# Performance work log

Measured on AMD Instinct MI355X. Metric: run time of the kernel, lower is better.

## Reference

```python
import jax, jax.numpy as jnp
import numpy as np

def setup_inputs() -> dict:
    key = jax.random.key(0)
    ks = jax.random.split(key, 8)
    B, C, H, W = 4, 64, 64, 64
    Cr = C // 8
    s = 1.0 / np.sqrt(C)
    return {
        "x": jax.random.normal(ks[0], (B, C, H, W), jnp.float32),
        "wq": jax.random.normal(ks[1], (Cr, C), jnp.float32) * s,
        "bq": jax.random.normal(ks[2], (Cr,), jnp.float32) * 0.01,
        "wk": jax.random.normal(ks[3], (Cr, C), jnp.float32) * s,
        "bk": jax.random.normal(ks[4], (Cr,), jnp.float32) * 0.01,
        "wv": jax.random.normal(ks[5], (C, C), jnp.float32) * s,
        "bv": jax.random.normal(ks[6], (C,), jnp.float32) * 0.01,
        "gamma": jax.random.normal(ks[7], (1,), jnp.float32) * 0.1,
    }

def reference(x, wq, bq, wk, bk, wv, bv, gamma):
    B, C, H, W = x.shape
    N = H * W
    xf = x.reshape(B, C, N)  # 1x1 conv == pointwise linear over channel dim
    q = jnp.einsum("oc,bcn->bno", wq, xf) + bq[None, None, :]   # (B, N, Cr)
    k = jnp.einsum("oc,bcn->bon", wk, xf) + bk[None, :, None]   # (B, Cr, N)
    v = jnp.einsum("oc,bcn->bon", wv, xf) + bv[None, :, None]   # (B, C, N)
    attn = jnp.einsum("bno,bom->bnm", q, k)                     # (B, N, N)
    attn = jax.nn.softmax(attn, axis=-1)
    out = jnp.einsum("bcm,bnm->bcn", v, attn)                   # (B, C, N)
    out = out.reshape(B, C, H, W)
    return x + gamma[0] * out
```

## Files before the change

### kernel.cpp

```cpp
#include <hip/hip_runtime.h>

#define BB 4
#define CC 64
#define NN 4096

typedef __attribute__((ext_vector_type(8))) short short8;
typedef __attribute__((ext_vector_type(4))) float f32x4;
typedef unsigned short u16;

#define QWS_ELEMS (BB * NN * 8)

__device__ inline u16 f2bf(float x) {
    unsigned u = __float_as_uint(x);
    u = (u + 0x7fffu + ((u >> 16) & 1u)) >> 16;
    return (u16)u;
}

__device__ inline unsigned permpack(float lo, float hi) {
    return __builtin_amdgcn_perm(__float_as_uint(hi), __float_as_uint(lo), 0x07060302);
}

__global__ __launch_bounds__(256) void proj_kernel(
    const float* __restrict__ x,
    const float* __restrict__ wq, const float* __restrict__ bq,
    const float* __restrict__ wk, const float* __restrict__ bk,
    const float* __restrict__ wv, const float* __restrict__ bv,
    u16* __restrict__ ws_u)
{
    u16* qws = ws_u;
    u16* kws = ws_u + QWS_ELEMS;
    u16* vws = ws_u + 2 * QWS_ELEMS;

    const int u   = blockIdx.y;
    const int pix = blockIdx.x * 256 + threadIdx.x;
    const int b   = pix >> 12;
    const int n   = pix & (NN - 1);

    const float* xb = x + ((size_t)b << 18) + n;

    float aq = bq[u], ak = bk[u];
    float av[8];
#pragma unroll
    for (int i = 0; i < 8; ++i) av[i] = bv[8 * u + i];

#pragma unroll 8
    for (int c = 0; c < CC; ++c) {
        const float xv = xb[(size_t)c << 12];
        aq += wq[u * CC + c] * xv;
        ak += wk[u * CC + c] * xv;
#pragma unroll
        for (int i = 0; i < 8; ++i)
            av[i] += wv[(8 * u + i) * CC + c] * xv;
    }

    qws[(size_t)pix * 8 + u] = f2bf(aq);
    kws[(size_t)pix * 8 + u] = f2bf(ak);
#pragma unroll
    for (int i = 0; i < 8; ++i)
        vws[(((size_t)((b << 6) + 8 * u + i)) << 12) + n] = f2bf(av[i]);
}

__global__ __launch_bounds__(256) void attn_kernel(
    const float* __restrict__ x, const float* __restrict__ gamma,
    const u16* __restrict__ ws_u, float* __restrict__ out)
{
    const u16* qws = ws_u;
    const u16* kws = ws_u + QWS_ELEMS;
    const u16* vws = ws_u + 2 * QWS_ELEMS;

    __shared__ u16   v_t[2][CC * 64];
    __shared__ u16   p_t[2][32 * 64];
    __shared__ float l_sh[4][32];

    const int tid  = threadIdx.x;
    const int w    = tid >> 6;
    const int lane = tid & 63;
    const int quad = lane >> 4;
    const int l15  = lane & 15;

    const int b  = blockIdx.y;
    const int qb = blockIdx.x << 5;
    const int bN = b << 12;

    short8 qf0 = {0,0,0,0,0,0,0,0}, qf1 = {0,0,0,0,0,0,0,0};
    if (quad == 0) {
        qf0 = *(const short8*)(qws + (size_t)(bN + qb + l15) * 8);
        qf1 = *(const short8*)(qws + (size_t)(bN + qb + 16 + l15) * 8);
    }

    short8 kf = {0,0,0,0,0,0,0,0};
    if (quad == 0)
        kf = *(const short8*)(kws + (size_t)(bN + (w << 4) + l15) * 8);

    const int c_row = tid >> 2;
    const int m4    = tid & 3;
    const u16* vrow = vws + (((size_t)((b << 6) + c_row)) << 12);
    short8 vpre0 = *(const short8*)(vrow + (m4 << 3));
    short8 vpre1 = *(const short8*)(vrow + 32 + (m4 << 3));

    const int sw  = c_row & 7;
    const int st0 = c_row * 64 + ((m4 ^ sw) << 3);
    const int st1 = c_row * 64 + (((m4 | 4) ^ sw) << 3);

    const int pm8  = (w << 1) + (quad >> 1);
    const int poff = (quad & 1) << 2;
    const int pw0  = l15 * 64        + ((pm8 ^ (l15 & 7)) << 3) + poff;
    const int pw1  = (16 + l15) * 64 + ((pm8 ^ ((16 + l15) & 7)) << 3) + poff;

    const int qc2   = w & 1;
    const int ch    = w >> 1;
    const int prow  = (qc2 << 4) + l15;
    const int crow0 = (ch << 5) + l15;
    const int crow1 = crow0 + 16;
    const int pr0 = prow * 64  + ((quad       ^ (prow & 7))  << 3);
    const int pr1 = prow * 64  + (((4 + quad) ^ (prow & 7))  << 3);
    const int v00 = crow0 * 64 + ((quad       ^ (crow0 & 7)) << 3);
    const int v01 = crow1 * 64 + ((quad       ^ (crow1 & 7)) << 3);
    const int v10 = crow0 * 64 + (((4 + quad) ^ (crow0 & 7)) << 3);
    const int v11 = crow1 * 64 + (((4 + quad) ^ (crow1 & 7)) << 3);

    f32x4 acc0 = {0.f, 0.f, 0.f, 0.f};
    f32x4 acc1 = {0.f, 0.f, 0.f, 0.f};
    float ls0 = 0.f, ls1 = 0.f;

    for (int it = 0; it < 64; ++it) {
        const int buf   = it & 1;
        const int mnext = ((it + 1) & 63) << 6;

        *(short8*)&v_t[buf][st0] = vpre0;
        *(short8*)&v_t[buf][st1] = vpre1;
        vpre0 = *(const short8*)(vrow + mnext + (m4 << 3));
        vpre1 = *(const short8*)(vrow + mnext + 32 + (m4 << 3));

        f32x4 s0 = __builtin_amdgcn_mfma_f32_16x16x32_bf16(
            kf, qf0, (f32x4){0.f,0.f,0.f,0.f}, 0, 0, 0);
        f32x4 s1 = __builtin_amdgcn_mfma_f32_16x16x32_bf16(
            kf, qf1, (f32x4){0.f,0.f,0.f,0.f}, 0, 0, 0);
        if (quad == 0)
            kf = *(const short8*)(kws + (size_t)(bN + mnext + (w << 4) + l15) * 8);

        const float p00 = __expf(s0[0]), p01 = __expf(s0[1]);
        const float p02 = __expf(s0[2]), p03 = __expf(s0[3]);
        const float p10 = __expf(s1[0]), p11 = __expf(s1[1]);
        const float p12 = __expf(s1[2]), p13 = __expf(s1[3]);
        ls0 += (p00 + p01) + (p02 + p03);
        ls1 += (p10 + p11) + (p12 + p13);
        uint2 a, c2;
        a.x  = permpack(p00, p01);  a.y  = permpack(p02, p03);
        c2.x = permpack(p10, p11);  c2.y = permpack(p12, p13);
        *(uint2*)&p_t[buf][pw0] = a;
        *(uint2*)&p_t[buf][pw1] = c2;

        __syncthreads();

        const short8 pf0  = *(const short8*)&p_t[buf][pr0];
        const short8 pf1  = *(const short8*)&p_t[buf][pr1];
        const short8 vf00 = *(const short8*)&v_t[buf][v00];
        const short8 vf01 = *(const short8*)&v_t[buf][v01];
        const short8 vf10 = *(const short8*)&v_t[buf][v10];
        const short8 vf11 = *(const short8*)&v_t[buf][v11];
        acc0 = __builtin_amdgcn_mfma_f32_16x16x32_bf16(pf0, vf00, acc0, 0, 0, 0);
        acc1 = __builtin_amdgcn_mfma_f32_16x16x32_bf16(pf0, vf01, acc1, 0, 0, 0);
        acc0 = __builtin_amdgcn_mfma_f32_16x16x32_bf16(pf1, vf10, acc0, 0, 0, 0);
        acc1 = __builtin_amdgcn_mfma_f32_16x16x32_bf16(pf1, vf11, acc1, 0, 0, 0);
    }

    ls0 += __shfl_xor(ls0, 16, 64); ls0 += __shfl_xor(ls0, 32, 64);
    ls1 += __shfl_xor(ls1, 16, 64); ls1 += __shfl_xor(ls1, 32, 64);
    if (quad == 0) { l_sh[w][l15] = ls0; l_sh[w][16 + l15] = ls1; }
    __syncthreads();

    const int q0 = (qc2 << 4) + (quad << 2);
    float rl[4];
#pragma unroll
    for (int r = 0; r < 4; ++r)
        rl[r] = 1.f / (l_sh[0][q0 + r] + l_sh[1][q0 + r] +
                       l_sh[2][q0 + r] + l_sh[3][q0 + r]);

    const float g = gamma[0];
#pragma unroll
    for (int half = 0; half < 2; ++half) {
        const int c = half ? crow1 : crow0;
        const f32x4 acc = half ? acc1 : acc0;
        const size_t base = (((size_t)((b << 6) + c)) << 12) + qb + q0;
        const float4 xv = *(const float4*)&x[base];
        float4 o;
        o.x = xv.x + g * acc[0] * rl[0];
        o.y = xv.y + g * acc[1] * rl[1];
        o.z = xv.z + g * acc[2] * rl[2];
        o.w = xv.w + g * acc[3] * rl[3];
        *(float4*)&out[base] = o;
    }
}

extern "C" void kernel_launch(void* const* d_in, const int* in_sizes, int n_in,
                              void* d_out, int out_size, void* d_ws, size_t ws_size,
                              hipStream_t stream)
{
    const float* x     = (const float*)d_in[0];
    const float* wq    = (const float*)d_in[1];
    const float* bq    = (const float*)d_in[2];
    const float* wk    = (const float*)d_in[3];
    const float* bk    = (const float*)d_in[4];
    const float* wv    = (const float*)d_in[5];
    const float* bv    = (const float*)d_in[6];
    const float* gamma = (const float*)d_in[7];
    u16*   ws  = (u16*)d_ws;
    float* out = (float*)d_out;

    hipLaunchKernelGGL(proj_kernel, dim3(BB * NN / 256, 8), dim3(256), 0, stream,
                       x, wq, bq, wk, bk, wv, bv, ws);
    hipLaunchKernelGGL(attn_kernel, dim3(NN / 32, BB), dim3(256), 0, stream,
                       x, gamma, ws, out);
}
```

Before: 112.3 us.

## Restructure projection per pixel and load V fragments directly from global in attention

The projection kernel now holds all 64 input channels of a pixel in registers and splits the output channels across the four wavefronts, with one wave doing q/k plus four v channels. This removes the 8x re-read of x across blockIdx.y and lets q/k be written as packed 16-byte stores. The attention kernel moves to 512 threads covering 64 queries, drops the V shared-memory staging and reads MFMA V fragments straight from global memory with a one-iteration prefetch. This raises occupancy pressure and makes V traffic depend on L2 hits rather than LDS reuse.

```diff
diff --git a/kernel.cpp b/kernel.cpp
--- a/kernel.cpp
+++ b/kernel.cpp
@@ -15,7 +15,9 @@
     u = (u + 0x7fffu + ((u >> 16) & 1u)) >> 16;
     return (u16)u;
 }
-
+__device__ inline unsigned pack2rne(float a, float b) {
+    return (unsigned)f2bf(a) | ((unsigned)f2bf(b) << 16);
+}
 __device__ inline unsigned permpack(float lo, float hi) {
     return __builtin_amdgcn_perm(__float_as_uint(hi), __float_as_uint(lo), 0x07060302);
 }
@@ -31,36 +33,63 @@
     u16* kws = ws_u + QWS_ELEMS;
     u16* vws = ws_u + 2 * QWS_ELEMS;
 
-    const int u   = blockIdx.y;
-    const int pix = blockIdx.x * 256 + threadIdx.x;
-    const int b   = pix >> 12;
-    const int n   = pix & (NN - 1);
-
+    const int part = __builtin_amdgcn_readfirstlane(threadIdx.x >> 6);
+    const int pix  = blockIdx.x * 64 + (threadIdx.x & 63);
+    const int b    = pix >> 12;
+    const int n    = pix & (NN - 1);
     const float* xb = x + ((size_t)b << 18) + n;
 
-    float aq = bq[u], ak = bk[u];
-    float av[8];
-#pragma unroll
-    for (int i = 0; i < 8; ++i) av[i] = bv[8 * u + i];
-
-#pragma unroll 8
-    for (int c = 0; c < CC; ++c) {
-        const float xv = xb[(size_t)c << 12];
-        aq += wq[u * CC + c] * xv;
-        ak += wk[u * CC + c] * xv;
-#pragma unroll
-        for (int i = 0; i < 8; ++i)
-            av[i] += wv[(8 * u + i) * CC + c] * xv;
-    }
-
-    qws[(size_t)pix * 8 + u] = f2bf(aq);
-    kws[(size_t)pix * 8 + u] = f2bf(ak);
-#pragma unroll
-    for (int i = 0; i < 8; ++i)
-        vws[(((size_t)((b << 6) + 8 * u + i)) << 12) + n] = f2bf(av[i]);
-}
-
-__global__ __launch_bounds__(256) void attn_kernel(
+    float xr[CC];
+#pragma unroll
+    for (int c = 0; c < CC; ++c) xr[c] = xb[(size_t)c << 12];
+
+    if (part == 0) {
+        float aq[8], ak[8], av[4];
+#pragma unroll
+        for (int i = 0; i < 8; ++i) { aq[i] = bq[i]; ak[i] = bk[i]; }
+#pragma unroll
+        for (int i = 0; i < 4; ++i) av[i] = bv[60 + i];
+#pragma unroll
+        for (int c = 0; c < CC; ++c) {
+            const float xv = xr[c];
+#pragma unroll
+            for (int i = 0; i < 8; ++i) {
+                aq[i] += wq[i * CC + c] * xv;
+                ak[i] += wk[i * CC + c] * xv;
+            }
+#pragma unroll
+            for (int i = 0; i < 4; ++i)
+                av[i] += wv[(60 + i) * CC + c] * xv;
+        }
+        uint4 qp, kp;
+        qp.x = pack2rne(aq[0], aq[1]); qp.y = pack2rne(aq[2], aq[3]);
+        qp.z = pack2rne(aq[4], aq[5]); qp.w = pack2rne(aq[6], aq[7]);
+        kp.x = pack2rne(ak[0], ak[1]); kp.y = pack2rne(ak[2], ak[3]);
+        kp.z = pack2rne(ak[4], ak[5]); kp.w = pack2rne(ak[6], ak[7]);
+        *(uint4*)&qws[(size_t)pix * 8] = qp;
+        *(uint4*)&kws[(size_t)pix * 8] = kp;
+#pragma unroll
+        for (int i = 0; i < 4; ++i)
+            vws[(((size_t)((b << 6) + 60 + i)) << 12) + n] = f2bf(av[i]);
+    } else {
+        const int o0 = (part - 1) * 20;
+        float av[20];
+#pragma unroll
+        for (int i = 0; i < 20; ++i) av[i] = bv[o0 + i];
+#pragma unroll
+        for (int c = 0; c < CC; ++c) {
+            const float xv = xr[c];
+#pragma unroll
+            for (int i = 0; i < 20; ++i)
+                av[i] += wv[(o0 + i) * CC + c] * xv;
+        }
+#pragma unroll
+        for (int i = 0; i < 20; ++i)
+            vws[(((size_t)((b << 6) + o0 + i)) << 12) + n] = f2bf(av[i]);
+    }
+}
+
+__global__ __launch_bounds__(512) void attn_kernel(
     const float* __restrict__ x, const float* __restrict__ gamma,
     const u16* __restrict__ ws_u, float* __restrict__ out)
 {
@@ -68,9 +97,8 @@
     const u16* kws = ws_u + QWS_ELEMS;
     const u16* vws = ws_u + 2 * QWS_ELEMS;
 
-    __shared__ u16   v_t[2][CC * 64];
-    __shared__ u16   p_t[2][32 * 64];
-    __shared__ float l_sh[4][32];
+    __shared__ u16   p_t[2][64 * 64];
+    __shared__ float l_sh[8][32];
 
     const int tid  = threadIdx.x;
     const int w    = tid >> 6;
@@ -79,45 +107,39 @@
     const int l15  = lane & 15;
 
     const int b  = blockIdx.y;
-    const int qb = blockIdx.x << 5;
+    const int qb = blockIdx.x << 6;
     const int bN = b << 12;
 
+    const int mc = w >> 1;
+    const int qh = w & 1;
+
     short8 qf0 = {0,0,0,0,0,0,0,0}, qf1 = {0,0,0,0,0,0,0,0};
+    short8 kf  = {0,0,0,0,0,0,0,0};
     if (quad == 0) {
-        qf0 = *(const short8*)(qws + (size_t)(bN + qb + l15) * 8);
-        qf1 = *(const short8*)(qws + (size_t)(bN + qb + 16 + l15) * 8);
-    }
-
-    short8 kf = {0,0,0,0,0,0,0,0};
-    if (quad == 0)
-        kf = *(const short8*)(kws + (size_t)(bN + (w << 4) + l15) * 8);
-
-    const int c_row = tid >> 2;
-    const int m4    = tid & 3;
-    const u16* vrow = vws + (((size_t)((b << 6) + c_row)) << 12);
-    short8 vpre0 = *(const short8*)(vrow + (m4 << 3));
-    short8 vpre1 = *(const short8*)(vrow + 32 + (m4 << 3));
-
-    const int sw  = c_row & 7;
-    const int st0 = c_row * 64 + ((m4 ^ sw) << 3);
-    const int st1 = c_row * 64 + (((m4 | 4) ^ sw) << 3);
-
-    const int pm8  = (w << 1) + (quad >> 1);
+        qf0 = *(const short8*)(qws + (size_t)(bN + qb + (qh << 5) + l15) * 8);
+        qf1 = *(const short8*)(qws + (size_t)(bN + qb + (qh << 5) + 16 + l15) * 8);
+        kf  = *(const short8*)(kws + (size_t)(bN + (mc << 4) + l15) * 8);
+    }
+
+    const int sw   = l15 & 7;
+    const int pm8  = (mc << 1) + (quad >> 1);
     const int poff = (quad & 1) << 2;
-    const int pw0  = l15 * 64        + ((pm8 ^ (l15 & 7)) << 3) + poff;
-    const int pw1  = (16 + l15) * 64 + ((pm8 ^ ((16 + l15) & 7)) << 3) + poff;
-
-    const int qc2   = w & 1;
-    const int ch    = w >> 1;
-    const int prow  = (qc2 << 4) + l15;
-    const int crow0 = (ch << 5) + l15;
-    const int crow1 = crow0 + 16;
-    const int pr0 = prow * 64  + ((quad       ^ (prow & 7))  << 3);
-    const int pr1 = prow * 64  + (((4 + quad) ^ (prow & 7))  << 3);
-    const int v00 = crow0 * 64 + ((quad       ^ (crow0 & 7)) << 3);
-    const int v01 = crow1 * 64 + ((quad       ^ (crow1 & 7)) << 3);
-    const int v10 = crow0 * 64 + (((4 + quad) ^ (crow0 & 7)) << 3);
-    const int v11 = crow1 * 64 + (((4 + quad) ^ (crow1 & 7)) << 3);
+    const int pw0  = ((qh << 5) + l15) * 64 + ((pm8 ^ sw) << 3) + poff;
+    const int pw1  = pw0 + (16 * 64);
+
+    const int qc   = w & 3;
+    const int ch   = w >> 2;
+    const int prow = (qc << 4) + l15;
+    const int pr0  = prow * 64 + ((quad ^ sw) << 3);
+    const int pr1  = prow * 64 + (((4 + quad) ^ sw) << 3);
+
+    const u16* vp0 = vws + (((size_t)((b << 6) + ((ch << 1) + 0) * 16 + l15)) << 12) + (quad << 3);
+    const u16* vp1 = vws + (((size_t)((b << 6) + ((ch << 1) + 1) * 16 + l15)) << 12) + (quad << 3);
+
+    short8 vf00 = *(const short8*)(vp0);
+    short8 vf01 = *(const short8*)(vp1);
+    short8 vf10 = *(const short8*)(vp0 + 32);
+    short8 vf11 = *(const short8*)(vp1 + 32);
 
     f32x4 acc0 = {0.f, 0.f, 0.f, 0.f};
     f32x4 acc1 = {0.f, 0.f, 0.f, 0.f};
@@ -126,18 +148,13 @@
     for (int it = 0; it < 64; ++it) {
         const int buf   = it & 1;
         const int mnext = ((it + 1) & 63) << 6;
-
-        *(short8*)&v_t[buf][st0] = vpre0;
-        *(short8*)&v_t[buf][st1] = vpre1;
-        vpre0 = *(const short8*)(vrow + mnext + (m4 << 3));
-        vpre1 = *(const short8*)(vrow + mnext + 32 + (m4 << 3));
 
         f32x4 s0 = __builtin_amdgcn_mfma_f32_16x16x32_bf16(
             kf, qf0, (f32x4){0.f,0.f,0.f,0.f}, 0, 0, 0);
         f32x4 s1 = __builtin_amdgcn_mfma_f32_16x16x32_bf16(
             kf, qf1, (f32x4){0.f,0.f,0.f,0.f}, 0, 0, 0);
         if (quad == 0)
-            kf = *(const short8*)(kws + (size_t)(bN + mnext + (w << 4) + l15) * 8);
+            kf = *(const short8*)(kws + (size_t)(bN + mnext + (mc << 4) + l15) * 8);
 
         const float p00 = __expf(s0[0]), p01 = __expf(s0[1]);
         const float p02 = __expf(s0[2]), p03 = __expf(s0[3]);
@@ -145,24 +162,25 @@
         const float p12 = __expf(s1[2]), p13 = __expf(s1[3]);
         ls0 += (p00 + p01) + (p02 + p03);
         ls1 += (p10 + p11) + (p12 + p13);
-        uint2 a, c2;
-        a.x  = permpack(p00, p01);  a.y  = permpack(p02, p03);
-        c2.x = permpack(p10, p11);  c2.y = permpack(p12, p13);
-        *(uint2*)&p_t[buf][pw0] = a;
-        *(uint2*)&p_t[buf][pw1] = c2;
+        uint2 a0, a1;
+        a0.x = permpack(p00, p01); a0.y = permpack(p02, p03);
+        a1.x = permpack(p10, p11); a1.y = permpack(p12, p13);
+        *(uint2*)&p_t[buf][pw0] = a0;
+        *(uint2*)&p_t[buf][pw1] = a1;
 
         __syncthreads();
 
-        const short8 pf0  = *(const short8*)&p_t[buf][pr0];
-        const short8 pf1  = *(const short8*)&p_t[buf][pr1];
-        const short8 vf00 = *(const short8*)&v_t[buf][v00];
-        const short8 vf01 = *(const short8*)&v_t[buf][v01];
-        const short8 vf10 = *(const short8*)&v_t[buf][v10];
-        const short8 vf11 = *(const short8*)&v_t[buf][v11];
+        const short8 pf0 = *(const short8*)&p_t[buf][pr0];
+        const short8 pf1 = *(const short8*)&p_t[buf][pr1];
         acc0 = __builtin_amdgcn_mfma_f32_16x16x32_bf16(pf0, vf00, acc0, 0, 0, 0);
         acc1 = __builtin_amdgcn_mfma_f32_16x16x32_bf16(pf0, vf01, acc1, 0, 0, 0);
         acc0 = __builtin_amdgcn_mfma_f32_16x16x32_bf16(pf1, vf10, acc0, 0, 0, 0);
         acc1 = __builtin_amdgcn_mfma_f32_16x16x32_bf16(pf1, vf11, acc1, 0, 0, 0);
+
+        vf00 = *(const short8*)(vp0 + mnext);
+        vf01 = *(const short8*)(vp1 + mnext);
+        vf10 = *(const short8*)(vp0 + mnext + 32);
+        vf11 = *(const short8*)(vp1 + mnext + 32);
     }
 
     ls0 += __shfl_xor(ls0, 16, 64); ls0 += __shfl_xor(ls0, 32, 64);
@@ -170,25 +188,26 @@
     if (quad == 0) { l_sh[w][l15] = ls0; l_sh[w][16 + l15] = ls1; }
     __syncthreads();
 
-    const int q0 = (qc2 << 4) + (quad << 2);
+    const int qhh = qc >> 1;
+    const int qq0 = ((qc & 1) << 4) + (quad << 2);
     float rl[4];
 #pragma unroll
     for (int r = 0; r < 4; ++r)
-        rl[r] = 1.f / (l_sh[0][q0 + r] + l_sh[1][q0 + r] +
-                       l_sh[2][q0 + r] + l_sh[3][q0 + r]);
+        rl[r] = 1.f / (l_sh[0 + qhh][qq0 + r] + l_sh[2 + qhh][qq0 + r] +
+                       l_sh[4 + qhh][qq0 + r] + l_sh[6 + qhh][qq0 + r]);
 
     const float g = gamma[0];
 #pragma unroll
-    for (int half = 0; half < 2; ++half) {
-        const int c = half ? crow1 : crow0;
-        const f32x4 acc = half ? acc1 : acc0;
-        const size_t base = (((size_t)((b << 6) + c)) << 12) + qb + q0;
+    for (int j = 0; j < 2; ++j) {
+        const int c = ((ch << 1) + j) * 16 + l15;
+        const f32x4 a = j ? acc1 : acc0;
+        const size_t base = (((size_t)((b << 6) + c)) << 12) + qb + (qc << 4) + (quad << 2);
         const float4 xv = *(const float4*)&x[base];
         float4 o;
-        o.x = xv.x + g * acc[0] * rl[0];
-        o.y = xv.y + g * acc[1] * rl[1];
-        o.z = xv.z + g * acc[2] * rl[2];
-        o.w = xv.w + g * acc[3] * rl[3];
+        o.x = xv.x + g * a[0] * rl[0];
+        o.y = xv.y + g * a[1] * rl[1];
+        o.z = xv.z + g * a[2] * rl[2];
+        o.w = xv.w + g * a[3] * rl[3];
         *(float4*)&out[base] = o;
     }
 }
@@ -208,8 +227,8 @@
     u16*   ws  = (u16*)d_ws;
     float* out = (float*)d_out;
 
-    hipLaunchKernelGGL(proj_kernel, dim3(BB * NN / 256, 8), dim3(256), 0, stream,
+    hipLaunchKernelGGL(proj_kernel, dim3(BB * NN / 64), dim3(256), 0, stream,
                        x, wq, bq, wk, bk, wv, bv, ws);
-    hipLaunchKernelGGL(attn_kernel, dim3(NN / 32, BB), dim3(256), 0, stream,
+    hipLaunchKernelGGL(attn_kernel, dim3(NN / 64, BB), dim3(512), 0, stream,
                        x, gamma, ws, out);
 }
```

After: 157.1 us. 1.4x slower.
